# Optimization experiments

Hardware: AMD Instinct MI355X
Metric: run time of the kernel (lower is better)

## Reference

```python
import jax, jax.numpy as jnp
import numpy as np

B, T, D_MODEL, HEAD_DIM = 4, 4096, 1024, 64

def setup_inputs() -> dict:
    key = jax.random.key(0)
    ks = jax.random.split(key, 7)
    s = 1.0 / np.sqrt(D_MODEL)
    return {
        "x": jax.random.normal(ks[0], (B, T, D_MODEL), dtype=jnp.float32),
        "Wq": jax.random.uniform(ks[1], (D_MODEL, HEAD_DIM), jnp.float32, -s, s),
        "bq": jax.random.uniform(ks[2], (HEAD_DIM,), jnp.float32, -s, s),
        "Wk": jax.random.uniform(ks[3], (D_MODEL, HEAD_DIM), jnp.float32, -s, s),
        "bk": jax.random.uniform(ks[4], (HEAD_DIM,), jnp.float32, -s, s),
        "Wv": jax.random.uniform(ks[5], (D_MODEL, HEAD_DIM), jnp.float32, -s, s),
        "bv": jax.random.uniform(ks[6], (HEAD_DIM,), jnp.float32, -s, s),
    }

def reference(x, Wq, bq, Wk, bk, Wv, bv):
    # x: [B,T,D]; projections -> [B,T,H]
    q = jnp.einsum("btd,dh->bth", x, Wq) + bq
    k = jnp.einsum("btd,dh->bth", x, Wk) + bk
    v = jnp.einsum("btd,dh->bth", x, Wv) + bv
    scale = HEAD_DIM ** -0.5
    # scores: [B,Tq,Tk] -- naive full attention matrix (memory-bound)
    scores = jnp.einsum("bqh,bkh->bqk", q, k) * scale
    neg = jnp.finfo(scores.dtype).min
    T_ = scores.shape[-1]
    causal = jnp.triu(jnp.full((T_, T_), neg, dtype=scores.dtype), k=1)
    scores = scores + causal[None, :, :]
    probs = jax.nn.softmax(scores, axis=-1)
    y = jnp.einsum("bqk,bkh->bqh", probs, v)
    return y
```

## Files before the change

### kernel.cpp

```cpp
#include <hip/hip_runtime.h>
#include <hip/hip_bf16.h>

typedef __attribute__((ext_vector_type(4))) float f4v;
typedef __attribute__((ext_vector_type(16))) float f16v;
typedef __attribute__((ext_vector_type(4))) unsigned short u16x4;
typedef __attribute__((ext_vector_type(8))) unsigned short u16x8;
typedef __attribute__((ext_vector_type(2))) unsigned int u32x2;
typedef __attribute__((ext_vector_type(4))) unsigned int u32x4;
typedef __attribute__((ext_vector_type(8))) __bf16 bf16x8;
typedef __attribute__((ext_vector_type(8))) _Float16 h8v;

#define D_MODEL 1024
#define HDIM 64
#define TSEQ 4096
#define QB 32
#define KVB 64
#define QSCALE 0.18033688011112042f

__device__ __forceinline__ unsigned short f2bf(float f) {
    union { float f; unsigned u; } v; v.f = f;
    unsigned r = v.u + 0x7FFFu + ((v.u >> 16) & 1u);
    return (unsigned short)(r >> 16);
}
__device__ __forceinline__ bf16x8 ld8(const unsigned short* p) {
    return __builtin_bit_cast(bf16x8, *(const u16x8*)p);
}
__device__ __forceinline__ h8v ldh8(const unsigned short* p) {
    return __builtin_bit_cast(h8v, *(const u16x8*)p);
}
__device__ __forceinline__ f4v mfma16f(h8v a, h8v b, f4v c) {
    return __builtin_amdgcn_mfma_f32_16x16x32_f16(a, b, c, 0, 0, 0);
}
__device__ __forceinline__ f16v mfma32(bf16x8 a, bf16x8 b, f16v c) {
    return __builtin_amdgcn_mfma_f32_32x32x16_bf16(a, b, c, 0, 0, 0);
}
__device__ __forceinline__ unsigned cvtpk(float a, float b) {
    unsigned r;
    asm("v_cvt_pk_bf16_f32 %0, %1, %2" : "=v"(r) : "v"(a), "v"(b));
    return r;
}
__device__ __forceinline__ void pswap(unsigned& a, unsigned& b) {
    asm("v_permlane32_swap_b32 %0, %1" : "+v"(a), "+v"(b));
}
__device__ __forceinline__ h8v pack8(f4v a, f4v b) {
    unsigned p0 = __builtin_bit_cast(unsigned, __builtin_amdgcn_cvt_pkrtz(a[0], a[1]));
    unsigned p1 = __builtin_bit_cast(unsigned, __builtin_amdgcn_cvt_pkrtz(a[2], a[3]));
    unsigned p2 = __builtin_bit_cast(unsigned, __builtin_amdgcn_cvt_pkrtz(b[0], b[1]));
    unsigned p3 = __builtin_bit_cast(unsigned, __builtin_amdgcn_cvt_pkrtz(b[2], b[3]));
    u32x4 u = {p0, p1, p2, p3};
    return __builtin_bit_cast(h8v, u);
}

__global__ void prep_wf(const float* __restrict__ Wq, const float* __restrict__ Wk,
                        const float* __restrict__ Wv, unsigned short* __restrict__ Wf)
{
    int idx = blockIdx.x * 256 + threadIdx.x;
    int j = idx & 7, lane = (idx >> 3) & 63, nf = (idx >> 9) & 3,
        kstep = (idx >> 11) & 31, m = idx >> 16;
    int k = kstep * 32 + 8 * (lane >> 4) + j;
    int n = nf * 16 + (lane & 15);
    const float* W = (m == 0) ? Wq : (m == 1) ? Wk : Wv;
    _Float16 hv = (_Float16)W[k * 64 + n];
    Wf[idx] = __builtin_bit_cast(unsigned short, hv);
}

__global__ __launch_bounds__(256, 2)
void proj_qkv(const float* __restrict__ x, const unsigned short* __restrict__ Wf,
              const float* __restrict__ bq, const float* __restrict__ bk,
              const float* __restrict__ bv,
              unsigned short* __restrict__ Qf, unsigned short* __restrict__ Kf,
              unsigned short* __restrict__ Vf)
{
    __shared__ float xs[2][4096];

    const int tid = threadIdx.x;
    const int w = tid >> 6, l = tid & 63;
    const int row0 = blockIdx.x * 32;

    f4v acc[2][3];
#pragma unroll
    for (int s = 0; s < 2; ++s)
#pragma unroll
        for (int f = 0; f < 3; ++f) acc[s][f] = (f4v)0.f;

    auto stage = [&](int buf, int t) {
#pragma unroll
        for (int i = 0; i < 4; ++i) {
            const int G0 = (i * 4 + w) * 64;
            const int G = G0 + l;
            const int row = G >> 5;
            const int gl = (G & 31) ^ (row & 7);
            const float* src = x + (size_t)(row0 + row) * D_MODEL + t * 128 + gl * 4;
            __builtin_amdgcn_global_load_lds(
                (const __attribute__((address_space(1))) unsigned*)src,
                (__attribute__((address_space(3))) unsigned*)&xs[buf][G0 * 4],
                16, 0, 0);
        }
    };

    stage(0, 0);
    __syncthreads();

#pragma unroll
    for (int t = 0; t < 8; ++t) {
        if (t < 7) stage((t + 1) & 1, t + 1);
        const int b = t & 1;
#pragma unroll
        for (int ks = 0; ks < 4; ++ks) {
            const int kglob = t * 4 + ks;
            h8v bw[3];
#pragma unroll
            for (int f = 0; f < 3; ++f) {
                const int cf = w * 3 + f;
                bw[f] = ldh8(Wf + ((((cf >> 2) * 32 + kglob) * 4 + (cf & 3)) << 9) + l * 8);
            }
            const int sw = l & 7;
            const int gr = ks * 8 + 2 * (l >> 4);
#pragma unroll
            for (int s = 0; s < 2; ++s) {
                const int row = s * 16 + (l & 15);
                f4v a0 = *(const f4v*)&xs[b][row * 128 + ((gr ^ sw) << 2)];
                f4v a1 = *(const f4v*)&xs[b][row * 128 + (((gr + 1) ^ sw) << 2)];
                h8v xa = pack8(a0, a1);
#pragma unroll
                for (int f = 0; f < 3; ++f)
                    acc[s][f] = mfma16f(xa, bw[f], acc[s][f]);
            }
        }
        __syncthreads();
    }

    const float* bias[3] = {bq, bk, bv};
#pragma unroll
    for (int s = 0; s < 2; ++s) {
        const int rowb = row0 + s * 16 + 4 * (l >> 4);
        const int b = rowb >> 12, tok0 = rowb & 4095;
#pragma unroll
        for (int f = 0; f < 3; ++f) {
            const int cf = w * 3 + f;
            const int m = cf >> 2, nf = cf & 3;
            const int d = nf * 16 + (l & 15);
            const float bb = bias[m][d];
            if (m == 0) {
                const int qtile = tok0 >> 5;
                const int ksq = d >> 4, hq = (d >> 3) & 1, jq = d & 7;
#pragma unroll
                for (int r4 = 0; r4 < 4; ++r4) {
                    int cq = (tok0 & 31) + r4;
                    Qf[(((size_t)(b * 128 + qtile) * 4 + ksq) << 9) + (32 * hq + cq) * 8 + jq] =
                        f2bf((acc[s][f][r4] + bb) * QSCALE);
                }
            } else if (m == 1) {
                const int t = tok0 >> 6, tb = (tok0 >> 5) & 1;
                const int ksk = d >> 4, hk = (d >> 3) & 1, jk = d & 7;
#pragma unroll
                for (int r4 = 0; r4 < 4; ++r4) {
                    int ck = (tok0 & 31) + r4;
                    Kf[(((size_t)((b * 64 + t) * 8 + tb * 4 + ksk)) << 9) + (32 * hk + ck) * 8 + jk] =
                        f2bf(acc[s][f][r4] + bb);
                }
            } else {
                const int t = tok0 >> 6, ku = (tok0 >> 4) & 3, hv = (tok0 >> 3) & 1, jv = tok0 & 7;
                const int cv = d & 31, td = d >> 5;
                u16x4 pk;
#pragma unroll
                for (int r4 = 0; r4 < 4; ++r4) pk[r4] = f2bf(acc[s][f][r4] + bb);
                *(u16x4*)(Vf + (((size_t)((b * 64 + t) * 8 + td * 4 + ku)) << 9) +
                          (32 * hv + cv) * 8 + jv) = pk;
            }
        }
    }
}

struct TState { float m, l; f16v o0, o1; };

__device__ __forceinline__ void run_tile(const unsigned short* __restrict__ Qf,
                                         const unsigned short* __restrict__ Kf,
                                         const unsigned short* __restrict__ Vf,
                                         int batch, int qt, int g8, int l, int h, int c,
                                         TState& st)
{
    const int NT = (qt >> 1) + 1;
    st.m = -1e30f; st.l = 0.f; st.o0 = (f16v)0.f; st.o1 = (f16v)0.f;

    bf16x8 qf[4];
    const unsigned short* qp = Qf + (((size_t)(batch * 128 + qt) * 4) << 9) + l * 8;
#pragma unroll
    for (int ks = 0; ks < 4; ++ks) qf[ks] = ld8(qp + (ks << 9));

    if (g8 >= NT) return;

    auto kload = [&](bf16x8(&kr)[2][4], int t_) {
        const unsigned short* p = Kf + (((size_t)(batch * 64 + t_) * 8) << 9) + l * 8;
#pragma unroll
        for (int tb = 0; tb < 2; ++tb)
#pragma unroll
            for (int ks = 0; ks < 4; ++ks)
                kr[tb][ks] = ld8(p + ((tb * 4 + ks) << 9));
    };

    auto body = [&](bf16x8(&kr)[2][4], bf16x8(&kn)[2][4], int t_) {
        bf16x8 vr[2][4];
        {
            const unsigned short* p = Vf + (((size_t)(batch * 64 + t_) * 8) << 9) + l * 8;
#pragma unroll
            for (int td = 0; td < 2; ++td)
#pragma unroll
                for (int ku = 0; ku < 4; ++ku)
                    vr[td][ku] = ld8(p + ((td * 4 + ku) << 9));
        }
        f16v sacc[2];
        sacc[0] = (f16v)0.f; sacc[1] = (f16v)0.f;
#pragma unroll
        for (int ks = 0; ks < 4; ++ks) {
            sacc[0] = mfma32(kr[0][ks], qf[ks], sacc[0]);
            sacc[1] = mfma32(kr[1][ks], qf[ks], sacc[1]);
        }
        int tn = t_ + 8; if (tn > NT - 1) tn = NT - 1;
        kload(kn, tn);
        if (t_ == NT - 1) {
            const int off = qt * QB - t_ * KVB;
#pragma unroll
            for (int tb = 0; tb < 2; ++tb)
#pragma unroll
                for (int r = 0; r < 16; ++r) {
                    int mv = 32 * tb + (r & 3) + 8 * (r >> 2) + 4 * h - off;
                    if (mv > c) sacc[tb][r] = -1e30f;
                }
        }
        float pm = -1e30f;
#pragma unroll
        for (int tb = 0; tb < 2; ++tb)
#pragma unroll
            for (int r = 0; r < 16; ++r) pm = fmaxf(pm, sacc[tb][r]);
        pm = fmaxf(pm, __shfl_xor(pm, 32));
        const float mnew = fmaxf(st.m, pm);
        const float sc = exp2f(st.m - mnew);
        st.m = mnew;
        float rs = 0.f;
        float p[2][16];
#pragma unroll
        for (int tb = 0; tb < 2; ++tb)
#pragma unroll
            for (int r = 0; r < 16; ++r) {
                float e = exp2f(sacc[tb][r] - mnew);
                p[tb][r] = e; rs += e;
            }
        rs += __shfl_xor(rs, 32);
        st.l = st.l * sc + rs;
#pragma unroll
        for (int r = 0; r < 16; ++r) { st.o0[r] *= sc; st.o1[r] *= sc; }
        bf16x8 pa[4];
#pragma unroll
        for (int tb = 0; tb < 2; ++tb) {
            unsigned wp[8];
#pragma unroll
            for (int i = 0; i < 8; ++i) wp[i] = cvtpk(p[tb][2 * i], p[tb][2 * i + 1]);
            pswap(wp[0], wp[2]); pswap(wp[1], wp[3]);
            pswap(wp[4], wp[6]); pswap(wp[5], wp[7]);
            u32x4 f0 = {wp[0], wp[1], wp[2], wp[3]};
            u32x4 f1 = {wp[4], wp[5], wp[6], wp[7]};
            pa[2 * tb]     = __builtin_bit_cast(bf16x8, f0);
            pa[2 * tb + 1] = __builtin_bit_cast(bf16x8, f1);
        }
#pragma unroll
        for (int ku = 0; ku < 4; ++ku) {
            st.o0 = mfma32(vr[0][ku], pa[ku], st.o0);
            st.o1 = mfma32(vr[1][ku], pa[ku], st.o1);
        }
    };

    bf16x8 kA[2][4], kB[2][4];
    int t = g8;
    kload(kA, t);
    for (;;) {
        body(kA, kB, t);
        t += 8; if (t >= NT) break;
        body(kB, kA, t);
        t += 8; if (t >= NT) break;
    }
}

__global__ __launch_bounds__(512, 2)
void attn(const unsigned short* __restrict__ Qf, const unsigned short* __restrict__ Kf,
          const unsigned short* __restrict__ Vf, float* __restrict__ Yg)
{
    __shared__ float Osm[8][QB][33];
    __shared__ float Msm[2][8][QB];
    __shared__ float Lsm[2][8][QB];

    const int tid = threadIdx.x;
    const int g8 = tid >> 6, l = tid & 63, h = l >> 5, c = l & 31;
    const int batch = blockIdx.x & 3;
    const int pr = blockIdx.x >> 2;
    const int qtA = pr, qtB = 127 - pr;

    TState sB, sA;
    run_tile(Qf, Kf, Vf, batch, qtB, g8, l, h, c, sB);
    run_tile(Qf, Kf, Vf, batch, qtA, g8, l, h, c, sA);

    if (h == 0) {
        Msm[0][g8][c] = sA.m; Lsm[0][g8][c] = sA.l;
        Msm[1][g8][c] = sB.m; Lsm[1][g8][c] = sB.l;
    }

    auto write_partial = [&](const f16v& o) {
#pragma unroll
        for (int r = 0; r < 16; ++r) {
            int dd = (r & 3) + 8 * (r >> 2) + 4 * h;
            Osm[g8][c][dd] = o[r];
        }
    };
    auto merge_phase = [&](int tile, int dhalf, int qt_) {
        const int q = tid >> 4, d2 = (tid & 15) * 2;
        float mm = -1e30f;
#pragma unroll
        for (int gg = 0; gg < 8; ++gg) mm = fmaxf(mm, Msm[tile][gg][q]);
        float L = 0.f, o0 = 0.f, o1 = 0.f;
#pragma unroll
        for (int gg = 0; gg < 8; ++gg) {
            float a = exp2f(Msm[tile][gg][q] - mm);
            L += a * Lsm[tile][gg][q];
            o0 += a * Osm[gg][q][d2];
            o1 += a * Osm[gg][q][d2 + 1];
        }
        float inv = 1.f / L;
        float* yp = Yg + ((size_t)batch * TSEQ + (size_t)qt_ * QB + q) * HDIM + dhalf * 32 + d2;
        yp[0] = o0 * inv; yp[1] = o1 * inv;
    };

    write_partial(sA.o0);
    __syncthreads();
    merge_phase(0, 0, qtA);
    __syncthreads();
    write_partial(sA.o1);
    __syncthreads();
    merge_phase(0, 1, qtA);
    __syncthreads();
    write_partial(sB.o0);
    __syncthreads();
    merge_phase(1, 0, qtB);
    __syncthreads();
    write_partial(sB.o1);
    __syncthreads();
    merge_phase(1, 1, qtB);
}

extern "C" void kernel_launch(void* const* d_in, const int* in_sizes, int n_in,
                              void* d_out, int out_size, void* d_ws, size_t ws_size,
                              hipStream_t stream)
{
    const float* x  = (const float*)d_in[0];
    const float* Wq = (const float*)d_in[1];
    const float* bq = (const float*)d_in[2];
    const float* Wk = (const float*)d_in[3];
    const float* bk = (const float*)d_in[4];
    const float* Wv = (const float*)d_in[5];
    const float* bv = (const float*)d_in[6];
    float* y = (float*)d_out;

    unsigned short* Qb = (unsigned short*)d_ws;
    unsigned short* Kb = Qb + (size_t)1048576;
    unsigned short* Vb = Kb + (size_t)1048576;
    unsigned short* Wf = Vb + (size_t)1048576;

    prep_wf<<<768, 256, 0, stream>>>(Wq, Wk, Wv, Wf);
    proj_qkv<<<512, 256, 0, stream>>>(x, Wf, bq, bk, bv, Qb, Kb, Vb);
    attn<<<256, 512, 0, stream>>>(Qb, Kb, Vb, y);
}
```

Measured before the change: 52.21 us.

## Pre-convert x to fp16 fragment layout and stage weights in LDS for projection

Adds a prep pass that converts x from fp32 to fp16 in MFMA fragment order, alongside the weight conversion, inside one fused prep kernel. The projection kernel then reads x fragments directly from global memory and stages only weight tiles through LDS. Each wave now owns a 16-row strip and six output column fragments, and each block covers half of the twelve fragments. The aim is to halve the x read bytes inside the projection and drop the in-loop fp32-to-fp16 packing, at the cost of an extra full write and read of x in fp16 through the workspace.

```diff
diff --git a/kernel.cpp b/kernel.cpp
--- a/kernel.cpp
+++ b/kernel.cpp
@@ -5,7 +5,6 @@
 typedef __attribute__((ext_vector_type(16))) float f16v;
 typedef __attribute__((ext_vector_type(4))) unsigned short u16x4;
 typedef __attribute__((ext_vector_type(8))) unsigned short u16x8;
-typedef __attribute__((ext_vector_type(2))) unsigned int u32x2;
 typedef __attribute__((ext_vector_type(4))) unsigned int u32x4;
 typedef __attribute__((ext_vector_type(8))) __bf16 bf16x8;
 typedef __attribute__((ext_vector_type(8))) _Float16 h8v;
@@ -51,49 +50,71 @@
     return __builtin_bit_cast(h8v, u);
 }
 
-__global__ void prep_wf(const float* __restrict__ Wq, const float* __restrict__ Wk,
-                        const float* __restrict__ Wv, unsigned short* __restrict__ Wf)
-{
-    int idx = blockIdx.x * 256 + threadIdx.x;
-    int j = idx & 7, lane = (idx >> 3) & 63, nf = (idx >> 9) & 3,
-        kstep = (idx >> 11) & 31, m = idx >> 16;
-    int k = kstep * 32 + 8 * (lane >> 4) + j;
-    int n = nf * 16 + (lane & 15);
-    const float* W = (m == 0) ? Wq : (m == 1) ? Wk : Wv;
-    _Float16 hv = (_Float16)W[k * 64 + n];
-    Wf[idx] = __builtin_bit_cast(unsigned short, hv);
+__global__ void fused_prep(const float* __restrict__ x, const float* __restrict__ Wq,
+                           const float* __restrict__ Wk, const float* __restrict__ Wv,
+                           unsigned short* __restrict__ Wf, unsigned short* __restrict__ xf)
+{
+    const int bid = blockIdx.x;
+    if (bid < 2048) {
+        const int gw = bid * 4 + (threadIdx.x >> 6);
+        const int l = threadIdx.x & 63;
+        const int row_l = l & 15, kc = l >> 4;
+#pragma unroll
+        for (int rep = 0; rep < 4; ++rep) {
+            const int u = gw + rep * 8192;
+            const int strip = u >> 5, kstep = u & 31;
+            const float* p = x + (size_t)(strip * 16 + row_l) * D_MODEL + kstep * 32 + 8 * kc;
+            f4v a = *(const f4v*)p;
+            f4v b = *(const f4v*)(p + 4);
+            h8v pk = pack8(a, b);
+            *(u16x8*)(xf + (((size_t)kstep * 1024 + strip) << 9) + l * 8) =
+                __builtin_bit_cast(u16x8, pk);
+        }
+    } else {
+        const int base = (bid - 2048) * 3072;
+#pragma unroll
+        for (int e = 0; e < 12; ++e) {
+            int idx = base + e * 256 + threadIdx.x;
+            int j = idx & 7, lane = (idx >> 3) & 63, nf = (idx >> 9) & 3,
+                kstep = (idx >> 11) & 31, m = idx >> 16;
+            int k = kstep * 32 + 8 * (lane >> 4) + j;
+            int n = nf * 16 + (lane & 15);
+            const float* W = (m == 0) ? Wq : (m == 1) ? Wk : Wv;
+            _Float16 hv = (_Float16)W[k * 64 + n];
+            Wf[idx] = __builtin_bit_cast(unsigned short, hv);
+        }
+    }
 }
 
 __global__ __launch_bounds__(256, 2)
-void proj_qkv(const float* __restrict__ x, const unsigned short* __restrict__ Wf,
-              const float* __restrict__ bq, const float* __restrict__ bk,
-              const float* __restrict__ bv,
-              unsigned short* __restrict__ Qf, unsigned short* __restrict__ Kf,
-              unsigned short* __restrict__ Vf)
-{
-    __shared__ float xs[2][4096];
+void projf(const unsigned short* __restrict__ xf, const unsigned short* __restrict__ Wf,
+           const float* __restrict__ bq, const float* __restrict__ bk,
+           const float* __restrict__ bv,
+           unsigned short* __restrict__ Qf, unsigned short* __restrict__ Kf,
+           unsigned short* __restrict__ Vf)
+{
+    __shared__ unsigned short wlds[2][6][4][512];
 
     const int tid = threadIdx.x;
     const int w = tid >> 6, l = tid & 63;
-    const int row0 = blockIdx.x * 32;
-
-    f4v acc[2][3];
-#pragma unroll
-    for (int s = 0; s < 2; ++s)
-#pragma unroll
-        for (int f = 0; f < 3; ++f) acc[s][f] = (f4v)0.f;
+    const int half = blockIdx.x & 1;
+    const int strip = (blockIdx.x >> 1) * 4 + w;
+
+    f4v acc[6];
+#pragma unroll
+    for (int f = 0; f < 6; ++f) acc[f] = (f4v)0.f;
 
     auto stage = [&](int buf, int t) {
 #pragma unroll
-        for (int i = 0; i < 4; ++i) {
-            const int G0 = (i * 4 + w) * 64;
-            const int G = G0 + l;
-            const int row = G >> 5;
-            const int gl = (G & 31) ^ (row & 7);
-            const float* src = x + (size_t)(row0 + row) * D_MODEL + t * 128 + gl * 4;
+        for (int j = 0; j < 6; ++j) {
+            const int ci = w * 6 + j;
+            const int f = ci >> 2, ks = ci & 3;
+            const int cf = half * 6 + f;
+            const unsigned short* src =
+                Wf + ((((cf >> 2) * 32 + (t * 4 + ks)) * 4 + (cf & 3)) << 9) + l * 8;
             __builtin_amdgcn_global_load_lds(
                 (const __attribute__((address_space(1))) unsigned*)src,
-                (__attribute__((address_space(3))) unsigned*)&xs[buf][G0 * 4],
+                (__attribute__((address_space(3))) unsigned*)&wlds[buf][f][ks][0],
                 16, 0, 0);
         }
     };
@@ -107,67 +128,51 @@
         const int b = t & 1;
 #pragma unroll
         for (int ks = 0; ks < 4; ++ks) {
-            const int kglob = t * 4 + ks;
-            h8v bw[3];
-#pragma unroll
-            for (int f = 0; f < 3; ++f) {
-                const int cf = w * 3 + f;
-                bw[f] = ldh8(Wf + ((((cf >> 2) * 32 + kglob) * 4 + (cf & 3)) << 9) + l * 8);
+            h8v xa = ldh8(xf + (((size_t)(t * 4 + ks) * 1024 + strip) << 9) + l * 8);
+#pragma unroll
+            for (int f = 0; f < 6; ++f) {
+                h8v bw = ldh8(&wlds[b][f][ks][l * 8]);
+                acc[f] = mfma16f(xa, bw, acc[f]);
             }
-            const int sw = l & 7;
-            const int gr = ks * 8 + 2 * (l >> 4);
-#pragma unroll
-            for (int s = 0; s < 2; ++s) {
-                const int row = s * 16 + (l & 15);
-                f4v a0 = *(const f4v*)&xs[b][row * 128 + ((gr ^ sw) << 2)];
-                f4v a1 = *(const f4v*)&xs[b][row * 128 + (((gr + 1) ^ sw) << 2)];
-                h8v xa = pack8(a0, a1);
-#pragma unroll
-                for (int f = 0; f < 3; ++f)
-                    acc[s][f] = mfma16f(xa, bw[f], acc[s][f]);
+        }
+        __syncthreads();
+    }
+
+    const float* bias[3] = {bq, bk, bv};
+    const int rowb = strip * 16 + 4 * (l >> 4);
+    const int b = rowb >> 12, tok0 = rowb & 4095;
+#pragma unroll
+    for (int f = 0; f < 6; ++f) {
+        const int cf = half * 6 + f;
+        const int m = cf >> 2, nf = cf & 3;
+        const int d = nf * 16 + (l & 15);
+        const float bb = bias[m][d];
+        if (m == 0) {
+            const int qtile = tok0 >> 5;
+            const int ksq = d >> 4, hq = (d >> 3) & 1, jq = d & 7;
+#pragma unroll
+            for (int r4 = 0; r4 < 4; ++r4) {
+                int cq = (tok0 & 31) + r4;
+                Qf[(((size_t)(b * 128 + qtile) * 4 + ksq) << 9) + (32 * hq + cq) * 8 + jq] =
+                    f2bf((acc[f][r4] + bb) * QSCALE);
             }
-        }
-        __syncthreads();
-    }
-
-    const float* bias[3] = {bq, bk, bv};
-#pragma unroll
-    for (int s = 0; s < 2; ++s) {
-        const int rowb = row0 + s * 16 + 4 * (l >> 4);
-        const int b = rowb >> 12, tok0 = rowb & 4095;
-#pragma unroll
-        for (int f = 0; f < 3; ++f) {
-            const int cf = w * 3 + f;
-            const int m = cf >> 2, nf = cf & 3;
-            const int d = nf * 16 + (l & 15);
-            const float bb = bias[m][d];
-            if (m == 0) {
-                const int qtile = tok0 >> 5;
-                const int ksq = d >> 4, hq = (d >> 3) & 1, jq = d & 7;
-#pragma unroll
-                for (int r4 = 0; r4 < 4; ++r4) {
-                    int cq = (tok0 & 31) + r4;
-                    Qf[(((size_t)(b * 128 + qtile) * 4 + ksq) << 9) + (32 * hq + cq) * 8 + jq] =
-                        f2bf((acc[s][f][r4] + bb) * QSCALE);
-                }
-            } else if (m == 1) {
-                const int t = tok0 >> 6, tb = (tok0 >> 5) & 1;
-                const int ksk = d >> 4, hk = (d >> 3) & 1, jk = d & 7;
-#pragma unroll
-                for (int r4 = 0; r4 < 4; ++r4) {
-                    int ck = (tok0 & 31) + r4;
-                    Kf[(((size_t)((b * 64 + t) * 8 + tb * 4 + ksk)) << 9) + (32 * hk + ck) * 8 + jk] =
-                        f2bf(acc[s][f][r4] + bb);
-                }
-            } else {
-                const int t = tok0 >> 6, ku = (tok0 >> 4) & 3, hv = (tok0 >> 3) & 1, jv = tok0 & 7;
-                const int cv = d & 31, td = d >> 5;
-                u16x4 pk;
-#pragma unroll
-                for (int r4 = 0; r4 < 4; ++r4) pk[r4] = f2bf(acc[s][f][r4] + bb);
-                *(u16x4*)(Vf + (((size_t)((b * 64 + t) * 8 + td * 4 + ku)) << 9) +
-                          (32 * hv + cv) * 8 + jv) = pk;
+        } else if (m == 1) {
+            const int t = tok0 >> 6, tb = (tok0 >> 5) & 1;
+            const int ksk = d >> 4, hk = (d >> 3) & 1, jk = d & 7;
+#pragma unroll
+            for (int r4 = 0; r4 < 4; ++r4) {
+                int ck = (tok0 & 31) + r4;
+                Kf[(((size_t)((b * 64 + t) * 8 + tb * 4 + ksk)) << 9) + (32 * hk + ck) * 8 + jk] =
+                    f2bf(acc[f][r4] + bb);
             }
+        } else {
+            const int t = tok0 >> 6, ku = (tok0 >> 4) & 3, hv = (tok0 >> 3) & 1, jv = tok0 & 7;
+            const int cv = d & 31, td = d >> 5;
+            u16x4 pk;
+#pragma unroll
+            for (int r4 = 0; r4 < 4; ++r4) pk[r4] = f2bf(acc[f][r4] + bb);
+            *(u16x4*)(Vf + (((size_t)((b * 64 + t) * 8 + td * 4 + ku)) << 9) +
+                      (32 * hv + cv) * 8 + jv) = pk;
         }
     }
 }
@@ -363,8 +368,9 @@
     unsigned short* Kb = Qb + (size_t)1048576;
     unsigned short* Vb = Kb + (size_t)1048576;
     unsigned short* Wf = Vb + (size_t)1048576;
-
-    prep_wf<<<768, 256, 0, stream>>>(Wq, Wk, Wv, Wf);
-    proj_qkv<<<512, 256, 0, stream>>>(x, Wf, bq, bk, bv, Qb, Kb, Vb);
+    unsigned short* xf = Wf + (size_t)262144;
+
+    fused_prep<<<2112, 256, 0, stream>>>(x, Wq, Wk, Wv, Wf, xf);
+    projf<<<512, 256, 0, stream>>>(xf, Wf, bq, bk, bv, Qb, Kb, Vb);
     attn<<<256, 512, 0, stream>>>(Qb, Kb, Vb, y);
 }
```

Result: slower. 59.26 us (+13.5%).

## Stage fp16-converted x and weight fragments in LDS for QKV projection

Applied to the files above, without the earlier changes.

Replaces the double-buffered async global_load_lds staging of fp32 x with a single-buffered scheme. Each thread loads fp32 x directly, converts it to fp16 once, and writes it to a padded LDS tile. The per-step weight fragments are also staged cooperatively through LDS instead of each wave reading them from global memory. The aim is to cut LDS footprint and redundant fp32-to-fp16 packing, but it gives up the async overlap of loads with MFMA and adds two barriers per k-step.

```diff
diff --git a/kernel.cpp b/kernel.cpp
--- a/kernel.cpp
+++ b/kernel.cpp
@@ -5,7 +5,6 @@
 typedef __attribute__((ext_vector_type(16))) float f16v;
 typedef __attribute__((ext_vector_type(4))) unsigned short u16x4;
 typedef __attribute__((ext_vector_type(8))) unsigned short u16x8;
-typedef __attribute__((ext_vector_type(2))) unsigned int u32x2;
 typedef __attribute__((ext_vector_type(4))) unsigned int u32x4;
 typedef __attribute__((ext_vector_type(8))) __bf16 bf16x8;
 typedef __attribute__((ext_vector_type(8))) _Float16 h8v;
@@ -71,11 +70,13 @@
               unsigned short* __restrict__ Qf, unsigned short* __restrict__ Kf,
               unsigned short* __restrict__ Vf)
 {
-    __shared__ float xs[2][4096];
+    __shared__ unsigned short xh[32][72];
+    __shared__ unsigned short wl[24][512];
 
     const int tid = threadIdx.x;
     const int w = tid >> 6, l = tid & 63;
     const int row0 = blockIdx.x * 32;
+    const int sr = tid >> 3, sc8 = (tid & 7) * 8;
 
     f4v acc[2][3];
 #pragma unroll
@@ -83,51 +84,42 @@
 #pragma unroll
         for (int f = 0; f < 3; ++f) acc[s][f] = (f4v)0.f;
 
-    auto stage = [&](int buf, int t) {
-#pragma unroll
-        for (int i = 0; i < 4; ++i) {
-            const int G0 = (i * 4 + w) * 64;
-            const int G = G0 + l;
-            const int row = G >> 5;
-            const int gl = (G & 31) ^ (row & 7);
-            const float* src = x + (size_t)(row0 + row) * D_MODEL + t * 128 + gl * 4;
-            __builtin_amdgcn_global_load_lds(
-                (const __attribute__((address_space(1))) unsigned*)src,
-                (__attribute__((address_space(3))) unsigned*)&xs[buf][G0 * 4],
-                16, 0, 0);
-        }
-    };
-
-    stage(0, 0);
-    __syncthreads();
-
-#pragma unroll
-    for (int t = 0; t < 8; ++t) {
-        if (t < 7) stage((t + 1) & 1, t + 1);
-        const int b = t & 1;
-#pragma unroll
-        for (int ks = 0; ks < 4; ++ks) {
-            const int kglob = t * 4 + ks;
+    const float* xp = x + (size_t)(row0 + sr) * D_MODEL + sc8;
+
+#pragma unroll
+    for (int t = 0; t < 16; ++t) {
+        __syncthreads();
+        {
+            f4v a0 = *(const f4v*)(xp + t * 64);
+            f4v a1 = *(const f4v*)(xp + t * 64 + 4);
+            h8v xa = pack8(a0, a1);
+            *(u16x8*)&xh[sr][sc8] = __builtin_bit_cast(u16x8, xa);
+        }
+#pragma unroll
+        for (int j = 0; j < 6; ++j) {
+            const int idx = j * 256 + tid;
+            const int chunk = idx >> 6;
+            const int cf = chunk >> 1, ks = chunk & 1;
+            const int lane = idx & 63;
+            *(u16x8*)&wl[chunk][lane * 8] =
+                *(const u16x8*)(Wf + ((((cf >> 2) * 32 + (t * 2 + ks)) * 4 + (cf & 3)) << 9)
+                                + lane * 8);
+        }
+        __syncthreads();
+#pragma unroll
+        for (int ks = 0; ks < 2; ++ks) {
             h8v bw[3];
 #pragma unroll
-            for (int f = 0; f < 3; ++f) {
-                const int cf = w * 3 + f;
-                bw[f] = ldh8(Wf + ((((cf >> 2) * 32 + kglob) * 4 + (cf & 3)) << 9) + l * 8);
+            for (int f = 0; f < 3; ++f)
+                bw[f] = ldh8(&wl[(w * 3 + f) * 2 + ks][l * 8]);
+#pragma unroll
+            for (int s = 0; s < 2; ++s) {
+                h8v xv = ldh8(&xh[s * 16 + (l & 15)][ks * 32 + 8 * (l >> 4)]);
+#pragma unroll
+                for (int f = 0; f < 3; ++f)
+                    acc[s][f] = mfma16f(xv, bw[f], acc[s][f]);
             }
-            const int sw = l & 7;
-            const int gr = ks * 8 + 2 * (l >> 4);
-#pragma unroll
-            for (int s = 0; s < 2; ++s) {
-                const int row = s * 16 + (l & 15);
-                f4v a0 = *(const f4v*)&xs[b][row * 128 + ((gr ^ sw) << 2)];
-                f4v a1 = *(const f4v*)&xs[b][row * 128 + (((gr + 1) ^ sw) << 2)];
-                h8v xa = pack8(a0, a1);
-#pragma unroll
-                for (int f = 0; f < 3; ++f)
-                    acc[s][f] = mfma16f(xa, bw[f], acc[s][f]);
-            }
-        }
-        __syncthreads();
+        }
     }
 
     const float* bias[3] = {bq, bk, bv};
```

Result: no change. 52.37 us (+0.3%).
